# Optimization experiments

Hardware: AMD Instinct MI355X
Metric: run time of the kernel (lower is better)

Reference implementation:

```python
import jax, jax.numpy as jnp
import numpy as np

B, T, C = 2, 2048, 2048
NH, NKV = 16, 4
HD = C // NH  # 128


def _rope(x, cos, sin):
    d = x.shape[-1] // 2
    x1, x2 = x[..., :d], x[..., d:]
    return jnp.concatenate([x1 * cos + x2 * sin, -x1 * sin + x2 * cos], axis=-1)


def _rmsnorm(x):
    eps = jnp.finfo(x.dtype).eps
    return x * jax.lax.rsqrt(jnp.mean(jnp.square(x), axis=-1, keepdims=True) + eps)


def setup_inputs() -> dict:
    key = jax.random.key(0)
    ks = jax.random.split(key, 7)
    s = 0.02
    return {
        "x": jax.random.normal(ks[0], (B, T, C), jnp.float32),
        "cos": jax.random.normal(ks[1], (1, T, 1, HD // 2), jnp.float32),
        "sin": jax.random.normal(ks[2], (1, T, 1, HD // 2), jnp.float32),
        "wq": jax.random.normal(ks[3], (C, NH * HD), jnp.float32) * s,
        "wk": jax.random.normal(ks[4], (C, NKV * HD), jnp.float32) * s,
        "wv": jax.random.normal(ks[5], (C, NKV * HD), jnp.float32) * s,
        "wo": jax.random.normal(ks[6], (C, C), jnp.float32) * s,
    }


def reference(x, cos, sin, wq, wk, wv, wo):
    q = (x @ wq).reshape(B, T, NH, HD)
    k = (x @ wk).reshape(B, T, NKV, HD)
    v = (x @ wv).reshape(B, T, NKV, HD)
    q = _rmsnorm(_rope(q, cos, sin))
    k = _rmsnorm(_rope(k, cos, sin))
    # [B, H, T, D]
    q = q.transpose(0, 2, 1, 3)
    k = k.transpose(0, 2, 1, 3)
    v = v.transpose(0, 2, 1, 3)
    rep = NH // NKV
    k = jnp.repeat(k, rep, axis=1)
    v = jnp.repeat(v, rep, axis=1)
    scale = 1.0 / jnp.sqrt(jnp.float32(HD))
    scores = jnp.einsum("bhqd,bhkd->bhqk", q, k) * scale
    causal = jnp.tril(jnp.ones((T, T), bool))
    scores = jnp.where(causal, scores, jnp.finfo(scores.dtype).min)
    attn = jax.nn.softmax(scores, axis=-1)
    y = jnp.einsum("bhqk,bhkd->bhqd", attn, v)
    y = y.transpose(0, 2, 1, 3).reshape(B, T, C)
    return y @ wo
```

## Files before the change

### kernel.cpp

```cpp
#include <hip/hip_runtime.h>
#include <hip/hip_bf16.h>
#include <cstdint>

typedef unsigned short u16;
typedef __bf16 bf16x8 __attribute__((ext_vector_type(8)));
typedef float f32x4 __attribute__((ext_vector_type(4)));
typedef unsigned short u16x8 __attribute__((ext_vector_type(8)));
typedef unsigned short u16x4 __attribute__((ext_vector_type(4)));

#define B_ 2
#define T_ 2048
#define C_ 2048
#define NH_ 16
#define NKV_ 4
#define HD_ 128
#define K2_ 0.12752004650581538f

__device__ __forceinline__ u16 f2bf(float f) {
    unsigned u = __builtin_bit_cast(unsigned, f);
    unsigned r = u + 0x7FFFu + ((u >> 16) & 1u);
    return (u16)(r >> 16);
}

__device__ __forceinline__ void gl16(const void* g, void* l) {
    auto gp = reinterpret_cast<const __attribute__((address_space(1))) unsigned*>(
        reinterpret_cast<uintptr_t>(g));
    auto lp = reinterpret_cast<__attribute__((address_space(3))) unsigned*>(
        reinterpret_cast<uintptr_t>(l));
    __builtin_amdgcn_global_load_lds(gp, lp, 16, 0, 0);
}

__global__ void transpose_conv(const float* __restrict__ in, u16* __restrict__ out, int N) {
    __shared__ float tile[32][33];
    int n0 = blockIdx.x * 32, k0 = blockIdx.y * 32;
    int tx = threadIdx.x, ty = threadIdx.y;
#pragma unroll
    for (int i = 0; i < 4; ++i)
        tile[ty * 4 + i][tx] = in[(size_t)(k0 + ty * 4 + i) * N + n0 + tx];
    __syncthreads();
#pragma unroll
    for (int i = 0; i < 4; ++i)
        out[(size_t)(n0 + ty * 4 + i) * 2048 + k0 + tx] = f2bf(tile[tx][ty * 4 + i]);
}

__global__ void convert4(const float4* __restrict__ in, u16* __restrict__ out) {
    int i = blockIdx.x * 256 + threadIdx.x;
    float4 v = in[i];
    u16x4 o;
    o[0] = f2bf(v.x); o[1] = f2bf(v.y); o[2] = f2bf(v.z); o[3] = f2bf(v.w);
    ((u16x4*)out)[i] = o;
}

__global__ __launch_bounds__(256, 2) void gemm_bf16(const u16* __restrict__ A,
                                                    const u16* __restrict__ BT,
                                                    float* __restrict__ C, int N, int K) {
    __shared__ __align__(16) u16 As[128 * 64];
    __shared__ __align__(16) u16 Bs[128 * 64];
    int t = threadIdx.x;
    int w = t >> 6, l = t & 63;
    int wr = w >> 1, wc = w & 1;
    int lg = l >> 4, lr = l & 15;
    int m0 = blockIdx.y * 128, n0 = blockIdx.x * 128;
    f32x4 acc[4][4] = {};

    int ar = t >> 3;
    int acb = (t & 7) * 16;
    const char* Abase = (const char*)(A + (size_t)(m0 + ar) * K) + acb;
    const char* Bbase = (const char*)(BT + (size_t)(n0 + ar) * K) + acb;
    char* AsB = (char*)As + t * 16;
    char* BsB = (char*)Bs + t * 16;

    for (int kt = 0; kt < K; kt += 64) {
        if (kt) __syncthreads();
#pragma unroll
        for (int i = 0; i < 4; ++i) {
            gl16(Abase + (size_t)(i * 32) * K * 2 + (size_t)kt * 2, AsB + i * 4096);
            gl16(Bbase + (size_t)(i * 32) * K * 2 + (size_t)kt * 2, BsB + i * 4096);
        }
        __syncthreads();
#pragma unroll
        for (int kk = 0; kk < 2; ++kk) {
            bf16x8 af[4], bfr[4];
#pragma unroll
            for (int m = 0; m < 4; ++m)
                af[m] = *(const bf16x8*)(As + (wr * 64 + m * 16 + lr) * 64 + kk * 32 + lg * 8);
#pragma unroll
            for (int n = 0; n < 4; ++n)
                bfr[n] = *(const bf16x8*)(Bs + (wc * 64 + n * 16 + lr) * 64 + kk * 32 + lg * 8);
#pragma unroll
            for (int m = 0; m < 4; ++m)
#pragma unroll
                for (int n = 0; n < 4; ++n)
                    acc[m][n] = __builtin_amdgcn_mfma_f32_16x16x32_bf16(af[m], bfr[n], acc[m][n], 0, 0, 0);
        }
    }
#pragma unroll
    for (int m = 0; m < 4; ++m) {
        int row = m0 + wr * 64 + m * 16 + lg * 4;
#pragma unroll
        for (int n = 0; n < 4; ++n) {
            int col = n0 + wc * 64 + n * 16 + lr;
            float* Cp = C + (size_t)row * N + col;
#pragma unroll
            for (int r = 0; r < 4; ++r)
                Cp[(size_t)r * N] = acc[m][n][r];
        }
    }
}

__global__ void rope_rms(const float* __restrict__ qkv, const float* __restrict__ cs,
                         const float* __restrict__ sn, u16* __restrict__ qh,
                         u16* __restrict__ kh) {
    int task = blockIdx.x * 4 + (threadIdx.x >> 6);
    int l = threadIdx.x & 63;
    const float* in;
    u16* out;
    int tpos;
    float post = 1.0f;
    if (task < 65536) {
        int row = task >> 4, h = task & 15;
        in = qkv + (size_t)row * 3072 + h * 128;
        int b = row >> 11; tpos = row & 2047;
        out = qh + ((size_t)(b * NH_ + h) * T_ + tpos) * HD_;
        post = K2_;
    } else {
        int t2 = task - 65536;
        int row = t2 >> 2, h = t2 & 3;
        in = qkv + (size_t)row * 3072 + 2048 + h * 128;
        int b = row >> 11; tpos = row & 2047;
        out = kh + ((size_t)(b * NKV_ + h) * T_ + tpos) * HD_;
    }
    float x1 = in[l], x2 = in[l + 64];
    float c = cs[tpos * 64 + l], s = sn[tpos * 64 + l];
    float o1 = x1 * c + x2 * s;
    float o2 = -x1 * s + x2 * c;
    float ss = o1 * o1 + o2 * o2;
#pragma unroll
    for (int m = 1; m < 64; m <<= 1) ss += __shfl_xor(ss, m);
    float r = rsqrtf(ss * (1.0f / 128.0f) + 1.1920929e-07f) * post;
    out[l] = f2bf(o1 * r);
    out[l + 64] = f2bf(o2 * r);
}

__global__ void transpose_v(const float* __restrict__ qkv, u16* __restrict__ vt) {
    __shared__ float tile[32][33];
    int t0 = blockIdx.x * 32;
    int d0 = blockIdx.y * 32;
    int bk = blockIdx.z;
    int b = bk >> 2, kvh = bk & 3;
    int tx = threadIdx.x, ty = threadIdx.y;
#pragma unroll
    for (int i = 0; i < 4; ++i)
        tile[ty * 4 + i][tx] =
            qkv[(size_t)(b * 2048 + t0 + ty * 4 + i) * 3072 + 2560 + kvh * 128 + d0 + tx];
    __syncthreads();
#pragma unroll
    for (int i = 0; i < 4; ++i)
        vt[((size_t)bk * 128 + d0 + ty * 4 + i) * 2048 + t0 + tx] = f2bf(tile[tx][ty * 4 + i]);
}

__global__ __launch_bounds__(512, 1) void attn(const u16* __restrict__ Q,
                                               const u16* __restrict__ Kk,
                                               const u16* __restrict__ V,
                                               u16* __restrict__ Y) {
    extern __shared__ __align__(16) u16 sm[];
    u16* Ks = sm;
    u16* Vs = sm + 16384;
    u16* Pb = sm + 32768;

    int bid = blockIdx.x;
    int xcd = bid & 7;
    int b = xcd >> 2, kvh = xcd & 3;
    int sp2 = bid >> 3;
    int t = threadIdx.x;
    int w = t >> 6, l = t & 63;
    int lg = l >> 4, lr = l & 15;
    int h = kvh * 4 + (w & 3);
    int j = sp2 * 2 + (w >> 2);
    int qwA = j * 16, qwB = (127 - j) * 16;
    int NA = j / 4 + 1;

    const u16* Qp = Q + (size_t)(b * NH_ + h) * T_ * HD_;
    const u16* Kp = Kk + (size_t)(b * NKV_ + kvh) * T_ * HD_;
    const u16* Vp = V + (size_t)(b * NKV_ + kvh) * HD_ * T_;
    u16* Yp = Y + (size_t)(b * T_) * 2048 + h * HD_;
    u16* Pw = Pb + w * 1152;

    int g0 = t, g1 = t + 512;
    auto stage = [&](int kv0, int buf) {
        const char* Kb = (const char*)Kp + (size_t)kv0 * 256;
        const char* Vb = (const char*)Vp + (size_t)kv0 * 2;
        char* Kd = (char*)(Ks + buf * 8192);
        char* Vd = (char*)(Vs + buf * 8192);
        gl16(Kb + (g0 >> 4) * 256 + (((g0 & 15) ^ ((g0 >> 4) & 15)) * 16), Kd + g0 * 16);
        gl16(Kb + (g1 >> 4) * 256 + (((g1 & 15) ^ ((g1 >> 4) & 15)) * 16), Kd + g1 * 16);
        gl16(Vb + (size_t)(g0 >> 3) * 4096 + (((g0 & 7) ^ ((g0 >> 3) & 7)) * 16), Vd + g0 * 16);
        gl16(Vb + (size_t)(g1 >> 3) * 4096 + (((g1 & 7) ^ ((g1 >> 3) & 7)) * 16), Vd + g1 * 16);
    };

    bf16x8 aq[4];
    auto loadQ = [&](int qw2) {
#pragma unroll
        for (int ch = 0; ch < 4; ++ch)
            aq[ch] = *(const bf16x8*)(Qp + (size_t)(qw2 + lr) * HD_ + ch * 32 + lg * 8);
    };

    f32x4 acc[8] = {};
    float m2[4], lp_[4];
#pragma unroll
    for (int r = 0; r < 4; ++r) { m2[r] = -1e30f; lp_[r] = 0.0f; }

    auto epi = [&](int qw2) {
#pragma unroll
        for (int r = 0; r < 4; ++r) {
            float lt = lp_[r];
            lt += __shfl_xor(lt, 1);
            lt += __shfl_xor(lt, 2);
            lt += __shfl_xor(lt, 4);
            lt += __shfl_xor(lt, 8);
            float inv = 1.0f / lt;
#pragma unroll
            for (int oc = 0; oc < 8; ++oc)
                Yp[(size_t)(qw2 + lg * 4 + r) * 2048 + oc * 16 + lr] = f2bf(acc[oc][r] * inv);
        }
    };

    loadQ(qwA);
    int qw = qwA;
    stage(0, 0);

    for (int gi = 0; gi < 33; ++gi) {
        asm volatile("s_waitcnt vmcnt(0)" ::: "memory");
        __builtin_amdgcn_s_barrier();
        __builtin_amdgcn_sched_barrier(0);
        int cur = gi & 1;
        if (gi < 32) {
            int gn = gi + 1;
            stage((gn < NA ? gn : gn - NA) * 64, cur ^ 1);
        }
        if (gi == NA) {
            epi(qwA);
#pragma unroll
            for (int oc = 0; oc < 8; ++oc) acc[oc] = f32x4{0.f, 0.f, 0.f, 0.f};
#pragma unroll
            for (int r = 0; r < 4; ++r) { m2[r] = -1e30f; lp_[r] = 0.0f; }
            loadQ(qwB);
            qw = qwB;
        }
        int kv0 = (gi < NA ? gi : gi - NA) * 64;
        int kbase = cur * 8192;

        f32x4 sc[4] = {};
        __builtin_amdgcn_s_setprio(1);
#pragma unroll
        for (int ch = 0; ch < 4; ++ch)
#pragma unroll
            for (int kf = 0; kf < 4; ++kf) {
                bf16x8 bk = *(const bf16x8*)&Ks[kbase + (kf * 16 + lr) * 128 + (((ch * 4 + lg) ^ lr) * 8)];
                sc[kf] = __builtin_amdgcn_mfma_f32_16x16x32_bf16(aq[ch], bk, sc[kf], 0, 0, 0);
            }
        __builtin_amdgcn_s_setprio(0);

        bf16x8 bv[16];
#pragma unroll
        for (int oc = 0; oc < 8; ++oc)
#pragma unroll
            for (int kk = 0; kk < 2; ++kk)
                bv[oc * 2 + kk] = *(const bf16x8*)&Vs[kbase + (oc * 16 + lr) * 64 +
                                                     (((kk * 4 + lg) ^ (lr & 7)) * 8)];

        bool nm = (kv0 + 63 >= qw);
        float sv[4][4], mx[4];
#pragma unroll
        for (int r = 0; r < 4; ++r) {
            int row = qw + lg * 4 + r;
#pragma unroll
            for (int kf = 0; kf < 4; ++kf) {
                float x = sc[kf][r];
                if (nm) {
                    int key = kv0 + kf * 16 + lr;
                    x = (key > row) ? -1e38f : x;
                }
                sv[r][kf] = x;
            }
            mx[r] = fmaxf(fmaxf(sv[r][0], sv[r][1]), fmaxf(sv[r][2], sv[r][3]));
        }
#pragma unroll
        for (int r = 0; r < 4; ++r) {
            float m = mx[r];
            m = fmaxf(m, __shfl_xor(m, 1));
            m = fmaxf(m, __shfl_xor(m, 2));
            m = fmaxf(m, __shfl_xor(m, 4));
            m = fmaxf(m, __shfl_xor(m, 8));
            mx[r] = m;
        }
        bool upd = false;
#pragma unroll
        for (int r = 0; r < 4; ++r) upd |= (mx[r] > m2[r] + 8.0f);
        if (__any(upd)) {
#pragma unroll
            for (int r = 0; r < 4; ++r) {
                float mn = fmaxf(m2[r], mx[r]);
                float rs = exp2f(m2[r] - mn);
                m2[r] = mn;
                lp_[r] *= rs;
#pragma unroll
                for (int oc = 0; oc < 8; ++oc) acc[oc] *= rs;
            }
        }
#pragma unroll
        for (int r = 0; r < 4; ++r) {
            float m = m2[r];
            float ps = 0.0f;
#pragma unroll
            for (int kf = 0; kf < 4; ++kf) {
                float p = exp2f(sv[r][kf] - m);
                ps += p;
                Pw[(lg * 4 + r) * 72 + kf * 16 + lr] = f2bf(p);
            }
            lp_[r] += ps;
        }
        bf16x8 ap[2];
#pragma unroll
        for (int kk = 0; kk < 2; ++kk)
            ap[kk] = *(const bf16x8*)&Pw[lr * 72 + kk * 32 + lg * 8];
        __builtin_amdgcn_s_setprio(1);
#pragma unroll
        for (int oc = 0; oc < 8; ++oc)
#pragma unroll
            for (int kk = 0; kk < 2; ++kk)
                acc[oc] = __builtin_amdgcn_mfma_f32_16x16x32_bf16(ap[kk], bv[oc * 2 + kk], acc[oc], 0, 0, 0);
        __builtin_amdgcn_s_setprio(0);
    }
    epi(qwB);
}

extern "C" void kernel_launch(void* const* d_in, const int* in_sizes, int n_in,
                              void* d_out, int out_size, void* d_ws, size_t ws_size,
                              hipStream_t stream) {
    const float* x    = (const float*)d_in[0];
    const float* cosT = (const float*)d_in[1];
    const float* sinT = (const float*)d_in[2];
    const float* wq   = (const float*)d_in[3];
    const float* wk   = (const float*)d_in[4];
    const float* wv   = (const float*)d_in[5];
    const float* wo   = (const float*)d_in[6];
    float* out = (float*)d_out;

    char* ws = (char*)d_ws;
    u16*   wqkvT = (u16*)(ws);
    u16*   woT   = (u16*)(ws + 12582912);
    u16*   xb    = (u16*)(ws + 20971520);
    float* qkv   = (float*)(ws + 37748736);
    u16*   qh    = (u16*)(ws + 88080384);
    u16*   kh    = (u16*)(ws + 104857600);
    u16*   vt    = (u16*)(ws + 109051904);
    u16*   y     = xb;

    static int smem_set = 0;
    if (!smem_set) {
        hipFuncSetAttribute(reinterpret_cast<const void*>(&attn),
                            hipFuncAttributeMaxDynamicSharedMemorySize, 83968);
        smem_set = 1;
    }

    transpose_conv<<<dim3(64, 64), dim3(32, 8), 0, stream>>>(wq, wqkvT, 2048);
    transpose_conv<<<dim3(16, 64), dim3(32, 8), 0, stream>>>(wk, wqkvT + (size_t)2048 * 2048, 512);
    transpose_conv<<<dim3(16, 64), dim3(32, 8), 0, stream>>>(wv, wqkvT + (size_t)2560 * 2048, 512);
    transpose_conv<<<dim3(64, 64), dim3(32, 8), 0, stream>>>(wo, woT, 2048);
    convert4<<<8192, 256, 0, stream>>>((const float4*)x, xb);

    gemm_bf16<<<dim3(24, 32), 256, 0, stream>>>(xb, wqkvT, qkv, 3072, 2048);

    rope_rms<<<20480, 256, 0, stream>>>(qkv, cosT, sinT, qh, kh);
    transpose_v<<<dim3(64, 4, 8), dim3(32, 8), 0, stream>>>(qkv, vt);

    attn<<<256, 512, 83968, stream>>>(qh, kh, vt, y);

    gemm_bf16<<<dim3(16, 32), 256, 0, stream>>>(y, woT, out, 2048, 2048);
}
```

Before: 236.7 us.

## Fuse RoPE and RMSNorm into QKV GEMM epilogue and restructure attention blocks

The QKV GEMM now applies RoPE and RMSNorm in its epilogue and writes bf16 Q/K head layouts directly. Only V goes out as fp32, into a narrower buffer. This removes the fp32 QKV round trip and the separate rope_rms launch. Attention changes from 512-thread blocks covering two query strips to 256-thread blocks with two blocks per CU. It also swaps the QK MFMA operand order so each lane holds a single query row, which simplifies the max and sum reductions. P is packed with v_cvt_pk_bf16_f32, and V fragments are loaded just before use instead of all up front. The fused epilogue adds shared-memory staging and barriers, and the attention change shifts occupancy and register pressure.

```diff
diff --git a/kernel.cpp b/kernel.cpp
--- a/kernel.cpp
+++ b/kernel.cpp
@@ -5,8 +5,8 @@
 typedef unsigned short u16;
 typedef __bf16 bf16x8 __attribute__((ext_vector_type(8)));
 typedef float f32x4 __attribute__((ext_vector_type(4)));
-typedef unsigned short u16x8 __attribute__((ext_vector_type(8)));
 typedef unsigned short u16x4 __attribute__((ext_vector_type(4)));
+typedef unsigned uint2v __attribute__((ext_vector_type(2)));
 
 #define B_ 2
 #define T_ 2048
@@ -20,6 +20,12 @@
     unsigned u = __builtin_bit_cast(unsigned, f);
     unsigned r = u + 0x7FFFu + ((u >> 16) & 1u);
     return (u16)(r >> 16);
+}
+
+__device__ __forceinline__ unsigned cvtpk(float a, float b) {
+    unsigned r;
+    asm("v_cvt_pk_bf16_f32 %0, %1, %2" : "=v"(r) : "v"(a), "v"(b));
+    return r;
 }
 
 __device__ __forceinline__ void gl16(const void* g, void* l) {
@@ -62,14 +68,12 @@
     int lg = l >> 4, lr = l & 15;
     int m0 = blockIdx.y * 128, n0 = blockIdx.x * 128;
     f32x4 acc[4][4] = {};
-
     int ar = t >> 3;
     int acb = (t & 7) * 16;
     const char* Abase = (const char*)(A + (size_t)(m0 + ar) * K) + acb;
     const char* Bbase = (const char*)(BT + (size_t)(n0 + ar) * K) + acb;
     char* AsB = (char*)As + t * 16;
     char* BsB = (char*)Bs + t * 16;
-
     for (int kt = 0; kt < K; kt += 64) {
         if (kt) __syncthreads();
 #pragma unroll
@@ -108,41 +112,127 @@
     }
 }
 
-__global__ void rope_rms(const float* __restrict__ qkv, const float* __restrict__ cs,
-                         const float* __restrict__ sn, u16* __restrict__ qh,
-                         u16* __restrict__ kh) {
-    int task = blockIdx.x * 4 + (threadIdx.x >> 6);
-    int l = threadIdx.x & 63;
-    const float* in;
-    u16* out;
-    int tpos;
-    float post = 1.0f;
-    if (task < 65536) {
-        int row = task >> 4, h = task & 15;
-        in = qkv + (size_t)row * 3072 + h * 128;
-        int b = row >> 11; tpos = row & 2047;
-        out = qh + ((size_t)(b * NH_ + h) * T_ + tpos) * HD_;
-        post = K2_;
-    } else {
-        int t2 = task - 65536;
-        int row = t2 >> 2, h = t2 & 3;
-        in = qkv + (size_t)row * 3072 + 2048 + h * 128;
-        int b = row >> 11; tpos = row & 2047;
-        out = kh + ((size_t)(b * NKV_ + h) * T_ + tpos) * HD_;
+__global__ __launch_bounds__(256, 2) void gemm_qkv(const u16* __restrict__ A,
+                                                   const u16* __restrict__ BT,
+                                                   const float* __restrict__ cs,
+                                                   const float* __restrict__ sn,
+                                                   u16* __restrict__ qh, u16* __restrict__ kh,
+                                                   float* __restrict__ vbuf) {
+    extern __shared__ __align__(16) char smu[];
+    u16* As = (u16*)smu;
+    u16* Bs = (u16*)(smu + 16384);
+    const int K = 2048;
+    int t = threadIdx.x;
+    int w = t >> 6, l = t & 63;
+    int wr = w >> 1, wc = w & 1;
+    int lg = l >> 4, lr = l & 15;
+    int m0 = blockIdx.y * 128, n0 = blockIdx.x * 128;
+    f32x4 acc[4][4] = {};
+    int ar = t >> 3;
+    int acb = (t & 7) * 16;
+    const char* Abase = (const char*)(A + (size_t)(m0 + ar) * K) + acb;
+    const char* Bbase = (const char*)(BT + (size_t)(n0 + ar) * K) + acb;
+    char* AsB = (char*)As + t * 16;
+    char* BsB = (char*)Bs + t * 16;
+    for (int kt = 0; kt < K; kt += 64) {
+        if (kt) __syncthreads();
+#pragma unroll
+        for (int i = 0; i < 4; ++i) {
+            gl16(Abase + (size_t)(i * 32) * K * 2 + (size_t)kt * 2, AsB + i * 4096);
+            gl16(Bbase + (size_t)(i * 32) * K * 2 + (size_t)kt * 2, BsB + i * 4096);
+        }
+        __syncthreads();
+#pragma unroll
+        for (int kk = 0; kk < 2; ++kk) {
+            bf16x8 af[4], bfr[4];
+#pragma unroll
+            for (int m = 0; m < 4; ++m)
+                af[m] = *(const bf16x8*)(As + (wr * 64 + m * 16 + lr) * 64 + kk * 32 + lg * 8);
+#pragma unroll
+            for (int n = 0; n < 4; ++n)
+                bfr[n] = *(const bf16x8*)(Bs + (wc * 64 + n * 16 + lr) * 64 + kk * 32 + lg * 8);
+#pragma unroll
+            for (int m = 0; m < 4; ++m)
+#pragma unroll
+                for (int n = 0; n < 4; ++n)
+                    acc[m][n] = __builtin_amdgcn_mfma_f32_16x16x32_bf16(af[m], bfr[n], acc[m][n], 0, 0, 0);
+        }
     }
-    float x1 = in[l], x2 = in[l + 64];
-    float c = cs[tpos * 64 + l], s = sn[tpos * 64 + l];
-    float o1 = x1 * c + x2 * s;
-    float o2 = -x1 * s + x2 * c;
-    float ss = o1 * o1 + o2 * o2;
-#pragma unroll
-    for (int m = 1; m < 64; m <<= 1) ss += __shfl_xor(ss, m);
-    float r = rsqrtf(ss * (1.0f / 128.0f) + 1.1920929e-07f) * post;
-    out[l] = f2bf(o1 * r);
-    out[l + 64] = f2bf(o2 * r);
-}
-
-__global__ void transpose_v(const float* __restrict__ qkv, u16* __restrict__ vt) {
+    int bx = blockIdx.x;
+    if (bx >= 20) {
+        int c0 = n0 - 2560 + wc * 64;
+#pragma unroll
+        for (int m = 0; m < 4; ++m) {
+            int row = m0 + wr * 64 + m * 16 + lg * 4;
+#pragma unroll
+            for (int n = 0; n < 4; ++n)
+#pragma unroll
+                for (int r = 0; r < 4; ++r)
+                    vbuf[(size_t)(row + r) * 512 + c0 + n * 16 + lr] = acc[m][n][r];
+        }
+        return;
+    }
+    __syncthreads();
+    float* ex = (float*)smu;
+    float* ssb = (float*)(smu + 67584);
+#pragma unroll
+    for (int m = 0; m < 4; ++m)
+#pragma unroll
+        for (int n = 0; n < 4; ++n)
+#pragma unroll
+            for (int r = 0; r < 4; ++r)
+                ex[(wr * 64 + m * 16 + lg * 4 + r) * 132 + wc * 64 + n * 16 + lr] = acc[m][n][r];
+    __syncthreads();
+#pragma unroll
+    for (int m = 0; m < 4; ++m)
+#pragma unroll
+        for (int n = 0; n < 4; ++n) {
+            int dlo = n * 16 + lr;
+#pragma unroll
+            for (int r = 0; r < 4; ++r) {
+                int row = wr * 64 + m * 16 + lg * 4 + r;
+                float x1 = ex[row * 132 + dlo];
+                float x2 = ex[row * 132 + 64 + dlo];
+                int tp = (m0 + row) & 2047;
+                float c = cs[tp * 64 + dlo];
+                float s = sn[tp * 64 + dlo];
+                acc[m][n][r] = (wc == 0) ? (x1 * c + x2 * s) : (x2 * c - x1 * s);
+            }
+        }
+#pragma unroll
+    for (int m = 0; m < 4; ++m)
+#pragma unroll
+        for (int r = 0; r < 4; ++r) {
+            float pa = 0.f;
+#pragma unroll
+            for (int n = 0; n < 4; ++n) pa += acc[m][n][r] * acc[m][n][r];
+            pa += __shfl_xor(pa, 1);
+            pa += __shfl_xor(pa, 2);
+            pa += __shfl_xor(pa, 4);
+            pa += __shfl_xor(pa, 8);
+            if (lr == 0) ssb[wc * 128 + wr * 64 + m * 16 + lg * 4 + r] = pa;
+        }
+    __syncthreads();
+    bool isQ = (bx < 16);
+#pragma unroll
+    for (int m = 0; m < 4; ++m)
+#pragma unroll
+        for (int r = 0; r < 4; ++r) {
+            int row = wr * 64 + m * 16 + lg * 4 + r;
+            float ssq = ssb[row] + ssb[128 + row];
+            float sc2 = rsqrtf(ssq * (1.0f / 128.0f) + 1.1920929e-07f);
+            if (isQ) sc2 *= K2_;
+            int gr = m0 + row;
+            int bb = gr >> 11, tp = gr & 2047;
+            u16* outp = isQ ? qh + ((size_t)(bb * NH_ + bx) * T_ + tp) * HD_
+                            : kh + ((size_t)(bb * NKV_ + (bx - 16)) * T_ + tp) * HD_;
+#pragma unroll
+            for (int n = 0; n < 4; ++n)
+                outp[wc * 64 + n * 16 + lr] = f2bf(acc[m][n][r] * sc2);
+        }
+}
+
+__global__ void transpose_v(const float* __restrict__ vbuf, u16* __restrict__ vt) {
     __shared__ float tile[32][33];
     int t0 = blockIdx.x * 32;
     int d0 = blockIdx.y * 32;
@@ -152,14 +242,14 @@
 #pragma unroll
     for (int i = 0; i < 4; ++i)
         tile[ty * 4 + i][tx] =
-            qkv[(size_t)(b * 2048 + t0 + ty * 4 + i) * 3072 + 2560 + kvh * 128 + d0 + tx];
+            vbuf[(size_t)(b * 2048 + t0 + ty * 4 + i) * 512 + kvh * 128 + d0 + tx];
     __syncthreads();
 #pragma unroll
     for (int i = 0; i < 4; ++i)
         vt[((size_t)bk * 128 + d0 + ty * 4 + i) * 2048 + t0 + tx] = f2bf(tile[tx][ty * 4 + i]);
 }
 
-__global__ __launch_bounds__(512, 1) void attn(const u16* __restrict__ Q,
+__global__ __launch_bounds__(256, 2) void attn(const u16* __restrict__ Q,
                                                const u16* __restrict__ Kk,
                                                const u16* __restrict__ V,
                                                u16* __restrict__ Y) {
@@ -171,12 +261,11 @@
     int bid = blockIdx.x;
     int xcd = bid & 7;
     int b = xcd >> 2, kvh = xcd & 3;
-    int sp2 = bid >> 3;
+    int j = bid >> 3;
     int t = threadIdx.x;
     int w = t >> 6, l = t & 63;
     int lg = l >> 4, lr = l & 15;
-    int h = kvh * 4 + (w & 3);
-    int j = sp2 * 2 + (w >> 2);
+    int h = kvh * 4 + w;
     int qwA = j * 16, qwB = (127 - j) * 16;
     int NA = j / 4 + 1;
 
@@ -186,16 +275,17 @@
     u16* Yp = Y + (size_t)(b * T_) * 2048 + h * HD_;
     u16* Pw = Pb + w * 1152;
 
-    int g0 = t, g1 = t + 512;
     auto stage = [&](int kv0, int buf) {
         const char* Kb = (const char*)Kp + (size_t)kv0 * 256;
         const char* Vb = (const char*)Vp + (size_t)kv0 * 2;
         char* Kd = (char*)(Ks + buf * 8192);
         char* Vd = (char*)(Vs + buf * 8192);
-        gl16(Kb + (g0 >> 4) * 256 + (((g0 & 15) ^ ((g0 >> 4) & 15)) * 16), Kd + g0 * 16);
-        gl16(Kb + (g1 >> 4) * 256 + (((g1 & 15) ^ ((g1 >> 4) & 15)) * 16), Kd + g1 * 16);
-        gl16(Vb + (size_t)(g0 >> 3) * 4096 + (((g0 & 7) ^ ((g0 >> 3) & 7)) * 16), Vd + g0 * 16);
-        gl16(Vb + (size_t)(g1 >> 3) * 4096 + (((g1 & 7) ^ ((g1 >> 3) & 7)) * 16), Vd + g1 * 16);
+#pragma unroll
+        for (int i = 0; i < 4; ++i) {
+            int g = t + i * 256;
+            gl16(Kb + (g >> 4) * 256 + (((g & 15) ^ ((g >> 4) & 15)) * 16), Kd + g * 16);
+            gl16(Vb + (size_t)(g >> 3) * 4096 + (((g & 7) ^ ((g >> 3) & 7)) * 16), Vd + g * 16);
+        }
     };
 
     bf16x8 aq[4];
@@ -206,23 +296,21 @@
     };
 
     f32x4 acc[8] = {};
-    float m2[4], lp_[4];
-#pragma unroll
-    for (int r = 0; r < 4; ++r) { m2[r] = -1e30f; lp_[r] = 0.0f; }
+    float m2 = -1e30f, lpS = 0.0f;
 
     auto epi = [&](int qw2) {
-#pragma unroll
-        for (int r = 0; r < 4; ++r) {
-            float lt = lp_[r];
-            lt += __shfl_xor(lt, 1);
-            lt += __shfl_xor(lt, 2);
-            lt += __shfl_xor(lt, 4);
-            lt += __shfl_xor(lt, 8);
-            float inv = 1.0f / lt;
-#pragma unroll
-            for (int oc = 0; oc < 8; ++oc)
-                Yp[(size_t)(qw2 + lg * 4 + r) * 2048 + oc * 16 + lr] = f2bf(acc[oc][r] * inv);
-        }
+        float lt = lpS;
+        lt += __shfl_xor(lt, 16);
+        lt += __shfl_xor(lt, 32);
+        float inv = 1.0f / lt;
+        float inv4[4];
+#pragma unroll
+        for (int r = 0; r < 4; ++r) inv4[r] = __shfl(inv, 4 * lg + r, 16);
+#pragma unroll
+        for (int oc = 0; oc < 8; ++oc)
+#pragma unroll
+            for (int r = 0; r < 4; ++r)
+                Yp[(size_t)(qw2 + 4 * lg + r) * 2048 + oc * 16 + lr] = f2bf(acc[oc][r] * inv4[r]);
     };
 
     loadQ(qwA);
@@ -242,8 +330,7 @@
             epi(qwA);
 #pragma unroll
             for (int oc = 0; oc < 8; ++oc) acc[oc] = f32x4{0.f, 0.f, 0.f, 0.f};
-#pragma unroll
-            for (int r = 0; r < 4; ++r) { m2[r] = -1e30f; lp_[r] = 0.0f; }
+            m2 = -1e30f; lpS = 0.0f;
             loadQ(qwB);
             qw = qwB;
         }
@@ -257,79 +344,71 @@
 #pragma unroll
             for (int kf = 0; kf < 4; ++kf) {
                 bf16x8 bk = *(const bf16x8*)&Ks[kbase + (kf * 16 + lr) * 128 + (((ch * 4 + lg) ^ lr) * 8)];
-                sc[kf] = __builtin_amdgcn_mfma_f32_16x16x32_bf16(aq[ch], bk, sc[kf], 0, 0, 0);
+                sc[kf] = __builtin_amdgcn_mfma_f32_16x16x32_bf16(bk, aq[ch], sc[kf], 0, 0, 0);
             }
         __builtin_amdgcn_s_setprio(0);
 
-        bf16x8 bv[16];
+        int qrow = qw + lr;
+        bool nm = (kv0 + 63 > qw);
+        if (nm) {
+#pragma unroll
+            for (int kf = 0; kf < 4; ++kf)
+#pragma unroll
+                for (int r = 0; r < 4; ++r) {
+                    int key = kv0 + kf * 16 + 4 * lg + r;
+                    if (key > qrow) sc[kf][r] = -1e38f;
+                }
+        }
+        float mk[4];
+#pragma unroll
+        for (int kf = 0; kf < 4; ++kf)
+            mk[kf] = fmaxf(fmaxf(sc[kf][0], sc[kf][1]), fmaxf(sc[kf][2], sc[kf][3]));
+        float mx = fmaxf(fmaxf(mk[0], mk[1]), fmaxf(mk[2], mk[3]));
+        mx = fmaxf(mx, __shfl_xor(mx, 16));
+        mx = fmaxf(mx, __shfl_xor(mx, 32));
+
+        if (__any(mx > m2 + 8.0f)) {
+            float mn = fmaxf(m2, mx);
+            float rs = exp2f(m2 - mn);
+            m2 = mn;
+            lpS *= rs;
+            float rs4[4];
+#pragma unroll
+            for (int r = 0; r < 4; ++r) rs4[r] = __shfl(rs, 4 * lg + r, 16);
+#pragma unroll
+            for (int oc = 0; oc < 8; ++oc)
+#pragma unroll
+                for (int r = 0; r < 4; ++r) acc[oc][r] *= rs4[r];
+        }
+
+        float ps = 0.0f;
+#pragma unroll
+        for (int kf = 0; kf < 4; ++kf) {
+            float p0 = exp2f(sc[kf][0] - m2);
+            float p1 = exp2f(sc[kf][1] - m2);
+            float p2 = exp2f(sc[kf][2] - m2);
+            float p3 = exp2f(sc[kf][3] - m2);
+            ps += (p0 + p1) + (p2 + p3);
+            uint2v pk;
+            pk[0] = cvtpk(p0, p1);
+            pk[1] = cvtpk(p2, p3);
+            *(uint2v*)&Pw[lr * 72 + kf * 16 + 4 * lg] = pk;
+        }
+        lpS += ps;
+
+        bf16x8 ap[2];
+#pragma unroll
+        for (int kk = 0; kk < 2; ++kk)
+            ap[kk] = *(const bf16x8*)&Pw[lr * 72 + kk * 32 + 8 * lg];
+        __builtin_amdgcn_s_setprio(1);
 #pragma unroll
         for (int oc = 0; oc < 8; ++oc)
 #pragma unroll
-            for (int kk = 0; kk < 2; ++kk)
-                bv[oc * 2 + kk] = *(const bf16x8*)&Vs[kbase + (oc * 16 + lr) * 64 +
-                                                     (((kk * 4 + lg) ^ (lr & 7)) * 8)];
-
-        bool nm = (kv0 + 63 >= qw);
-        float sv[4][4], mx[4];
-#pragma unroll
-        for (int r = 0; r < 4; ++r) {
-            int row = qw + lg * 4 + r;
-#pragma unroll
-            for (int kf = 0; kf < 4; ++kf) {
-                float x = sc[kf][r];
-                if (nm) {
-                    int key = kv0 + kf * 16 + lr;
-                    x = (key > row) ? -1e38f : x;
-                }
-                sv[r][kf] = x;
+            for (int kk = 0; kk < 2; ++kk) {
+                bf16x8 bv = *(const bf16x8*)&Vs[kbase + (oc * 16 + lr) * 64 +
+                                                (((kk * 4 + lg) ^ (lr & 7)) * 8)];
+                acc[oc] = __builtin_amdgcn_mfma_f32_16x16x32_bf16(ap[kk], bv, acc[oc], 0, 0, 0);
             }
-            mx[r] = fmaxf(fmaxf(sv[r][0], sv[r][1]), fmaxf(sv[r][2], sv[r][3]));
-        }
-#pragma unroll
-        for (int r = 0; r < 4; ++r) {
-            float m = mx[r];
-            m = fmaxf(m, __shfl_xor(m, 1));
-            m = fmaxf(m, __shfl_xor(m, 2));
-            m = fmaxf(m, __shfl_xor(m, 4));
-            m = fmaxf(m, __shfl_xor(m, 8));
-            mx[r] = m;
-        }
-        bool upd = false;
-#pragma unroll
-        for (int r = 0; r < 4; ++r) upd |= (mx[r] > m2[r] + 8.0f);
-        if (__any(upd)) {
-#pragma unroll
-            for (int r = 0; r < 4; ++r) {
-                float mn = fmaxf(m2[r], mx[r]);
-                float rs = exp2f(m2[r] - mn);
-                m2[r] = mn;
-                lp_[r] *= rs;
-#pragma unroll
-                for (int oc = 0; oc < 8; ++oc) acc[oc] *= rs;
-            }
-        }
-#pragma unroll
-        for (int r = 0; r < 4; ++r) {
-            float m = m2[r];
-            float ps = 0.0f;
-#pragma unroll
-            for (int kf = 0; kf < 4; ++kf) {
-                float p = exp2f(sv[r][kf] - m);
-                ps += p;
-                Pw[(lg * 4 + r) * 72 + kf * 16 + lr] = f2bf(p);
-            }
-            lp_[r] += ps;
-        }
-        bf16x8 ap[2];
-#pragma unroll
-        for (int kk = 0; kk < 2; ++kk)
-            ap[kk] = *(const bf16x8*)&Pw[lr * 72 + kk * 32 + lg * 8];
-        __builtin_amdgcn_s_setprio(1);
-#pragma unroll
-        for (int oc = 0; oc < 8; ++oc)
-#pragma unroll
-            for (int kk = 0; kk < 2; ++kk)
-                acc[oc] = __builtin_amdgcn_mfma_f32_16x16x32_bf16(ap[kk], bv[oc * 2 + kk], acc[oc], 0, 0, 0);
         __builtin_amdgcn_s_setprio(0);
     }
     epi(qwB);
@@ -351,18 +430,16 @@
     u16*   wqkvT = (u16*)(ws);
     u16*   woT   = (u16*)(ws + 12582912);
     u16*   xb    = (u16*)(ws + 20971520);
-    float* qkv   = (float*)(ws + 37748736);
+    float* vbuf  = (float*)(ws + 37748736);
     u16*   qh    = (u16*)(ws + 88080384);
     u16*   kh    = (u16*)(ws + 104857600);
     u16*   vt    = (u16*)(ws + 109051904);
     u16*   y     = xb;
 
-    static int smem_set = 0;
-    if (!smem_set) {
-        hipFuncSetAttribute(reinterpret_cast<const void*>(&attn),
-                            hipFuncAttributeMaxDynamicSharedMemorySize, 83968);
-        smem_set = 1;
-    }
+    hipFuncSetAttribute(reinterpret_cast<const void*>(&gemm_qkv),
+                        hipFuncAttributeMaxDynamicSharedMemorySize, 68608);
+    hipFuncSetAttribute(reinterpret_cast<const void*>(&attn),
+                        hipFuncAttributeMaxDynamicSharedMemorySize, 74752);
 
     transpose_conv<<<dim3(64, 64), dim3(32, 8), 0, stream>>>(wq, wqkvT, 2048);
     transpose_conv<<<dim3(16, 64), dim3(32, 8), 0, stream>>>(wk, wqkvT + (size_t)2048 * 2048, 512);
@@ -370,12 +447,11 @@
     transpose_conv<<<dim3(64, 64), dim3(32, 8), 0, stream>>>(wo, woT, 2048);
     convert4<<<8192, 256, 0, stream>>>((const float4*)x, xb);
 
-    gemm_bf16<<<dim3(24, 32), 256, 0, stream>>>(xb, wqkvT, qkv, 3072, 2048);
-
-    rope_rms<<<20480, 256, 0, stream>>>(qkv, cosT, sinT, qh, kh);
-    transpose_v<<<dim3(64, 4, 8), dim3(32, 8), 0, stream>>>(qkv, vt);
-
-    attn<<<256, 512, 83968, stream>>>(qh, kh, vt, y);
+    gemm_qkv<<<dim3(24, 32), 256, 68608, stream>>>(xb, wqkvT, cosT, sinT, qh, kh, vbuf);
+
+    transpose_v<<<dim3(64, 4, 8), dim3(32, 8), 0, stream>>>(vbuf, vt);
+
+    attn<<<512, 256, 74752, stream>>>(qh, kh, vt, y);
 
     gemm_bf16<<<dim3(16, 32), 256, 0, stream>>>(y, woT, out, 2048, 2048);
 }
```

Measured after the change: 291.4 us. +23.1%, slower.
